# Optimization experiments

Measured on AMD Instinct MI355X. Metric: run time of the kernel, lower is better.

The kernel has to match this reference:

```python
import jax, jax.numpy as jnp
import numpy as np

N_NODES = 50000
N_EDGES = 800000
K_HOPS = 3


def setup_inputs() -> dict:
    key = jax.random.key(0)
    ks = jax.random.split(key, 8)
    x = jax.random.normal(ks[0], (N_NODES, 56), dtype=jnp.float32)
    edge_index = jax.random.randint(ks[1], (2, N_EDGES), 0, N_NODES, dtype=jnp.int64)
    def glorot(k, shape):
        fan_in, fan_out = shape
        s = (6.0 / (fan_in + fan_out)) ** 0.5
        return jax.random.uniform(k, shape, jnp.float32, -s, s)
    return {
        "x": x,
        "edge_index": edge_index,
        "W1": glorot(ks[2], (56, 64)), "b1": jnp.zeros((64,), jnp.float32),
        "W2": glorot(ks[3], (64, 64)), "b2": jnp.zeros((64,), jnp.float32),
        "W3": glorot(ks[4], (64, 64)), "b3": jnp.zeros((64,), jnp.float32),
        "W4": glorot(ks[5], (64, 256)), "b4": jnp.zeros((256,), jnp.float32),
    }


def _gcn_norm(edge_index, num_nodes, dtype):
    # add self loops (PyG SGConv default), then symmetric D^{-1/2}(A+I)D^{-1/2} weights
    loop = jnp.arange(num_nodes, dtype=edge_index.dtype)
    src = jnp.concatenate([edge_index[0], loop])
    dst = jnp.concatenate([edge_index[1], loop])
    deg = jax.ops.segment_sum(jnp.ones_like(src, dtype=dtype), dst, num_segments=num_nodes)
    dinv = jnp.where(deg > 0, jax.lax.rsqrt(deg), 0.0).astype(dtype)
    norm = dinv[src] * dinv[dst]  # [E + N]
    return src, dst, norm


def _propagate_k(h, src, dst, norm, num_nodes, k):
    # k hops of sparse gather-scale-scatter: h <- A_hat @ h
    for _ in range(k):
        h = jax.ops.segment_sum(h[src] * norm[:, None], dst, num_segments=num_nodes)
    return h


def reference(x, edge_index, W1, b1, W2, b2, W3, b3, W4, b4):
    n = x.shape[0]
    src, dst, norm = _gcn_norm(edge_index, n, x.dtype)
    # SGConv layers (dropout is identity in eval mode)
    h = _propagate_k(x, src, dst, norm, n, K_HOPS) @ W1 + b1
    h = _propagate_k(h, src, dst, norm, n, K_HOPS) @ W2 + b2
    h = _propagate_k(h, src, dst, norm, n, K_HOPS) @ W3 + b3
    return h @ W4 + b4  # [N, output]
```

## Files before the change

### kernel.cpp

```cpp
#include <hip/hip_runtime.h>

#define N_NODES 50000
#define N_EDGES 800000
#define F_IN 56
#define F_PAD 64
#define F_OUT 256
#define NB 32
#define ELL_W 64
#define SEG_SZ 6250
#define ZROW N_NODES


__global__ __launch_bounds__(256) void k_fill(const int* __restrict__ ei,
                                              int* __restrict__ cnt,
                                              int* __restrict__ ell) {
  int seg = blockIdx.x & 7;
  int chunk = blockIdx.x >> 3;
  int nchunks = gridDim.x >> 3;
  int stride = nchunks * blockDim.x;
  for (int e = chunk * blockDim.x + threadIdx.x; e < N_EDGES; e += stride) {
    int d = ei[N_EDGES + e];
    if (d / SEG_SZ == seg) {
      int s = ei[e];
      int pos = atomicAdd(&cnt[d], 1);
      ell[(d << 6) + pos] = s;
    }
  }
}


__global__ void k_prep(const int* __restrict__ cnt, float* __restrict__ dinv,
                       float* __restrict__ ideg, float* __restrict__ sqd,
                       int* __restrict__ deg, int* __restrict__ ell) {
  int i = blockIdx.x * blockDim.x + threadIdx.x;
  if (i >= N_NODES) return;
  int c = cnt[i] + 1;
  float fc = (float)c;
  dinv[i] = rsqrtf(fc);
  ideg[i] = 1.0f / fc;
  sqd[i]  = sqrtf(fc);
  deg[i] = c;
  ell[(i << 6) + (c - 1)] = i;
}


__global__ void k_loadx(const float* __restrict__ x, const float* __restrict__ dinv,
                        float* __restrict__ h) {
  int i = blockIdx.x * blockDim.x + threadIdx.x;
  int nn = i >> 6, f = i & 63;
  float di = dinv[nn];
  float v = 0.f;
  if (f < F_IN) v = x[nn * F_IN + f] * di;
  else if (f == F_IN) v = di;
  h[i] = v;
}


__global__ __launch_bounds__(256) void k_hop(const float* __restrict__ hin,
                                             float* __restrict__ hout,
                                             const int* __restrict__ deg,
                                             const int* __restrict__ ell,
                                             const float* __restrict__ ideg,
                                             float* __restrict__ vsave) {
  int node = (blockIdx.x * blockDim.x + threadIdx.x) >> 6;
  int lane = threadIdx.x & 63;
  int d = __builtin_amdgcn_readfirstlane(deg[node]);
  int rec = ell[((size_t)node << 6) + lane];
  rec = (lane < d) ? rec : ZROW;
  float idg = __int_as_float(__builtin_amdgcn_readfirstlane(
      __float_as_int(ideg[node])));

  int sub = lane >> 4;
  int fo  = (lane & 15) << 2;
  float4 acc = make_float4(0.f, 0.f, 0.f, 0.f);

  int ngroups = (d + 3) >> 2;
  int g = 0;
  for (; g + 4 <= ngroups; g += 4) {
    int s0 = __shfl(rec, g * 4 + sub);
    int s1 = __shfl(rec, g * 4 + 4 + sub);
    int s2 = __shfl(rec, g * 4 + 8 + sub);
    int s3 = __shfl(rec, g * 4 + 12 + sub);
    float4 a0 = *(const float4*)(hin + (((size_t)s0) << 6) + fo);
    float4 a1 = *(const float4*)(hin + (((size_t)s1) << 6) + fo);
    float4 a2 = *(const float4*)(hin + (((size_t)s2) << 6) + fo);
    float4 a3 = *(const float4*)(hin + (((size_t)s3) << 6) + fo);
    acc.x += (a0.x + a1.x) + (a2.x + a3.x);
    acc.y += (a0.y + a1.y) + (a2.y + a3.y);
    acc.z += (a0.z + a1.z) + (a2.z + a3.z);
    acc.w += (a0.w + a1.w) + (a2.w + a3.w);
  }
  for (; g < ngroups; ++g) {
    int s0 = __shfl(rec, g * 4 + sub);
    float4 a0 = *(const float4*)(hin + (((size_t)s0) << 6) + fo);
    acc.x += a0.x; acc.y += a0.y; acc.z += a0.z; acc.w += a0.w;
  }
  acc.x += __shfl_xor(acc.x, 16);
  acc.y += __shfl_xor(acc.y, 16);
  acc.z += __shfl_xor(acc.z, 16);
  acc.w += __shfl_xor(acc.w, 16);
  acc.x += __shfl_xor(acc.x, 32);
  acc.y += __shfl_xor(acc.y, 32);
  acc.z += __shfl_xor(acc.z, 32);
  acc.w += __shfl_xor(acc.w, 32);

  acc.x *= idg; acc.y *= idg; acc.z *= idg; acc.w *= idg;

  if (lane < 16) {
    *(float4*)(hout + ((size_t)node << 6) + fo) = acc;
  }
  if (vsave != nullptr && lane == 14) vsave[node] = acc.x;
}


__global__ void k_weights(const float* __restrict__ W1, const float* __restrict__ b1,
                          const float* __restrict__ W2, const float* __restrict__ b2,
                          const float* __restrict__ W3, const float* __restrict__ b3,
                          const float* __restrict__ W4, const float* __restrict__ b4,
                          float* __restrict__ Mw, float* __restrict__ c1,
                          float* __restrict__ c2, float* __restrict__ c3) {
  __shared__ float t1[64], t2[64], t3[64];
  int m = blockIdx.x, tid = threadIdx.x;
  if (m < F_IN) {
    if (tid < 64) {
      float a = 0.f;
      for (int k = 0; k < 64; ++k) a = fmaf(W1[m * 64 + k], W2[k * 64 + tid], a);
      t1[tid] = a;
    }
    __syncthreads();
    if (tid < 64) {
      float a = 0.f;
      for (int k = 0; k < 64; ++k) a = fmaf(t1[k], W3[k * 64 + tid], a);
      t2[tid] = a;
    }
    __syncthreads();
    {
      float a = 0.f;
      for (int k = 0; k < 64; ++k) a = fmaf(t2[k], W4[k * 256 + tid], a);
      Mw[m * 256 + tid] = a;
    }
  } else {
    if (tid < 64) {
      float a = 0.f;
      for (int k = 0; k < 64; ++k) a = fmaf(b1[k], W2[k * 64 + tid], a);
      t1[tid] = a;
    }
    __syncthreads();
    if (tid < 64) {
      float a = 0.f, b = 0.f;
      for (int k = 0; k < 64; ++k) {
        float w3 = W3[k * 64 + tid];
        a = fmaf(t1[k], w3, a);
        b = fmaf(b2[k], w3, b);
      }
      t2[tid] = a; t3[tid] = b;
    }
    __syncthreads();
    {
      float a = 0.f, b = 0.f, c = 0.f;
      for (int k = 0; k < 64; ++k) {
        float w4 = W4[k * 256 + tid];
        a = fmaf(t2[k], w4, a);
        b = fmaf(t3[k], w4, b);
        c = fmaf(b3[k], w4, c);
      }
      c1[tid] = a; c2[tid] = b; c3[tid] = c + b4[tid];
    }
  }
}


__global__ __launch_bounds__(256) void k_final(const float* __restrict__ y,
                                               const float* __restrict__ v3u,
                                               const float* __restrict__ v6u,
                                               const float* __restrict__ sqd,
                                               const float* __restrict__ Mw,
                                               const float* __restrict__ c1,
                                               const float* __restrict__ c2,
                                               const float* __restrict__ c3,
                                               float* __restrict__ out) {
  __shared__ float4 yl[NB][16];
  __shared__ float v3l[NB], v6l[NB];
  int tid = threadIdx.x;
  int j = tid;

  float4 Mreg[14];
#pragma unroll
  for (int k4 = 0; k4 < 14; ++k4) {
    Mreg[k4].x = Mw[(k4 * 4 + 0) * F_OUT + j];
    Mreg[k4].y = Mw[(k4 * 4 + 1) * F_OUT + j];
    Mreg[k4].z = Mw[(k4 * 4 + 2) * F_OUT + j];
    Mreg[k4].w = Mw[(k4 * 4 + 3) * F_OUT + j];
  }
  float C1 = c1[j], C2 = c2[j], C3 = c3[j];

  int n0 = blockIdx.x * NB;
  int lim = min(NB, N_NODES - n0);
  for (int i = tid; i < lim * 16; i += 256) {
    int nn = i >> 4, q = i & 15;
    float sq = sqd[n0 + nn];
    float4 v = *(const float4*)(y + ((size_t)(n0 + nn) << 6) + q * 4);
    v.x *= sq; v.y *= sq; v.z *= sq; v.w *= sq;
    yl[nn][q] = v;
  }
  if (tid < lim) {
    float sq = sqd[n0 + tid];
    v3l[tid] = v3u[n0 + tid] * sq;
    v6l[tid] = v6u[n0 + tid] * sq;
  }
  __syncthreads();

  for (int nn = 0; nn < lim; ++nn) {
    float a0 = fmaf(v6l[nn], C1, fmaf(v3l[nn], C2, C3));
    float a1 = 0.f, a2 = 0.f, a3 = 0.f;
#pragma unroll
    for (int k4 = 0; k4 < 14; ++k4) {
      float4 yv = yl[nn][k4];
      a0 = fmaf(yv.x, Mreg[k4].x, a0);
      a1 = fmaf(yv.y, Mreg[k4].y, a1);
      a2 = fmaf(yv.z, Mreg[k4].z, a2);
      a3 = fmaf(yv.w, Mreg[k4].w, a3);
    }
    out[(size_t)(n0 + nn) * F_OUT + j] = (a0 + a1) + (a2 + a3);
  }
}


extern "C" void kernel_launch(void* const* d_in, const int* in_sizes, int n_in,
                              void* d_out, int out_size, void* d_ws, size_t ws_size,
                              hipStream_t stream) {
  const float* x  = (const float*)d_in[0];
  const int*   ei = (const int*)d_in[1];
  const float* W1 = (const float*)d_in[2];
  const float* b1 = (const float*)d_in[3];
  const float* W2 = (const float*)d_in[4];
  const float* b2 = (const float*)d_in[5];
  const float* W3 = (const float*)d_in[6];
  const float* b3 = (const float*)d_in[7];
  const float* W4 = (const float*)d_in[8];
  const float* b4 = (const float*)d_in[9];
  float* out = (float*)d_out;

  char* ws = (char*)d_ws;
  size_t off = 0;
  auto take = [&](size_t bytes) -> void* {
    void* p = ws + off;
    off += (bytes + 255) & ~(size_t)255;
    return p;
  };
  int*   cnt   = (int*)take((size_t)N_NODES * 4);
  int*   deg   = (int*)take((size_t)N_NODES * 4);
  float* dinv  = (float*)take((size_t)N_NODES * 4);
  float* ideg  = (float*)take((size_t)N_NODES * 4);
  float* sqd   = (float*)take((size_t)N_NODES * 4);
  float* v3    = (float*)take((size_t)N_NODES * 4);
  float* v6    = (float*)take((size_t)N_NODES * 4);
  int*   ell   = (int*)take((size_t)N_NODES * ELL_W * 4);
  float* hA    = (float*)take((size_t)(N_NODES + 1) * F_PAD * 4);
  float* hB    = (float*)take((size_t)(N_NODES + 1) * F_PAD * 4);
  float* Mw    = (float*)take((size_t)F_IN * F_OUT * 4);
  float* c1    = (float*)take((size_t)F_OUT * 4);
  float* c2    = (float*)take((size_t)F_OUT * 4);
  float* c3    = (float*)take((size_t)F_OUT * 4);

  (void)hipMemsetAsync(cnt, 0, (size_t)N_NODES * 4, stream);
  (void)hipMemsetAsync(hA + (size_t)ZROW * F_PAD, 0, F_PAD * 4, stream);
  (void)hipMemsetAsync(hB + (size_t)ZROW * F_PAD, 0, F_PAD * 4, stream);
  k_fill<<<1024, 256, 0, stream>>>(ei, cnt, ell);
  k_prep<<<(N_NODES + 255) / 256, 256, 0, stream>>>(cnt, dinv, ideg, sqd, deg, ell);
  k_loadx<<<(N_NODES * F_PAD) / 256, 256, 0, stream>>>(x, dinv, hA);
  k_weights<<<F_IN + 1, 256, 0, stream>>>(W1, b1, W2, b2, W3, b3, W4, b4, Mw, c1, c2, c3);

  float* src = hA;
  float* dst = hB;
  for (int hop = 1; hop <= 9; ++hop) {
    float* vs = (hop == 3) ? v3 : (hop == 6) ? v6 : nullptr;
    k_hop<<<(N_NODES * F_PAD) / 256, 256, 0, stream>>>(src, dst, deg, ell, ideg, vs);
    float* t = src; src = dst; dst = t;
  }
  k_final<<<(N_NODES + NB - 1) / NB, 256, 0, stream>>>(src, v3, v6, sqd, Mw, c1, c2, c3, out);
}
```

Measured before the change: 363.3 us.

## Group four destination nodes per wavefront with sorted shared ELL lists

The per-node ELL layout (one wavefront per node, 64 slots) becomes a per-group layout in which four consecutive destination nodes share a 128-slot list. Each entry is tagged with its local destination, and a wavefront bitonic sort orders the entries by source. The hop kernel has one wavefront process a whole group, using all four 16-lane subgroups on useful edges instead of leaving padded lanes idle for low-degree nodes. Masked FMAs route each gathered row into four accumulators. This cuts wavefront count and wasted gathers, at the cost of four times the accumulate math, extra shuffle reductions, and a sort preprocessing pass.

```diff
diff --git a/kernel.cpp b/kernel.cpp
--- a/kernel.cpp
+++ b/kernel.cpp
@@ -2,18 +2,20 @@
 
 #define N_NODES 50000
 #define N_EDGES 800000
+#define N_GROUPS 12500
+#define GSLOTS 128
 #define F_IN 56
 #define F_PAD 64
 #define F_OUT 256
 #define NB 32
-#define ELL_W 64
 #define SEG_SZ 6250
 #define ZROW N_NODES
+#define PAD_E 0x7FFFFFFF
 
 
 __global__ __launch_bounds__(256) void k_fill(const int* __restrict__ ei,
-                                              int* __restrict__ cnt,
-                                              int* __restrict__ ell) {
+                                              int* __restrict__ gcnt,
+                                              int* __restrict__ ellg) {
   int seg = blockIdx.x & 7;
   int chunk = blockIdx.x >> 3;
   int nchunks = gridDim.x >> 3;
@@ -22,25 +24,74 @@
     int d = ei[N_EDGES + e];
     if (d / SEG_SZ == seg) {
       int s = ei[e];
-      int pos = atomicAdd(&cnt[d], 1);
-      ell[(d << 6) + pos] = s;
-    }
-  }
-}
-
-
-__global__ void k_prep(const int* __restrict__ cnt, float* __restrict__ dinv,
-                       float* __restrict__ ideg, float* __restrict__ sqd,
-                       int* __restrict__ deg, int* __restrict__ ell) {
+      int g = d >> 2;
+      int pos = atomicAdd(&gcnt[g], 1);
+      ellg[(g << 7) + pos] = (s << 2) | (d & 3);
+    }
+  }
+}
+
+
+__global__ void k_self(int* __restrict__ gcnt, int* __restrict__ ellg) {
   int i = blockIdx.x * blockDim.x + threadIdx.x;
   if (i >= N_NODES) return;
-  int c = cnt[i] + 1;
-  float fc = (float)c;
-  dinv[i] = rsqrtf(fc);
-  ideg[i] = 1.0f / fc;
-  sqd[i]  = sqrtf(fc);
-  deg[i] = c;
-  ell[(i << 6) + (c - 1)] = i;
+  int g = i >> 2;
+  int pos = atomicAdd(&gcnt[g], 1);
+  ellg[(g << 7) + pos] = (i << 2) | (i & 3);
+}
+
+
+__global__ __launch_bounds__(256) void k_sort(const int* __restrict__ gcnt,
+                                              int* __restrict__ ellg,
+                                              float* __restrict__ dinv,
+                                              float* __restrict__ ideg,
+                                              float* __restrict__ sqd) {
+  int w = (blockIdx.x * blockDim.x + threadIdx.x) >> 6;
+  int l = threadIdx.x & 63;
+  int cnt = __builtin_amdgcn_readfirstlane(gcnt[w]);
+  int* base = ellg + ((size_t)w << 7);
+  int v0 = (l < cnt) ? base[l] : PAD_E;
+  int v1 = (64 + l < cnt) ? base[64 + l] : PAD_E;
+
+#pragma unroll
+  for (int k = 2; k <= 128; k <<= 1) {
+#pragma unroll
+    for (int j = 64; j > 0; j >>= 1) {
+      if (j >= k) continue;
+      if (j == 64) {
+        int lo = min(v0, v1), hi = max(v0, v1);
+        v0 = lo; v1 = hi;
+      } else {
+        int o0 = __shfl_xor(v0, j);
+        int o1 = __shfl_xor(v1, j);
+        bool lower = ((l & j) == 0);
+        bool up0 = ((l & k) == 0);
+        bool up1 = (((l + 64) & k) == 0);
+        v0 = (lower == up0) ? min(v0, o0) : max(v0, o0);
+        v1 = (lower == up1) ? min(v1, o1) : max(v1, o1);
+      }
+    }
+  }
+
+  int c0 = __popcll(__ballot(v0 != PAD_E && (v0 & 3) == 0)) +
+           __popcll(__ballot(v1 != PAD_E && (v1 & 3) == 0));
+  int c1 = __popcll(__ballot(v0 != PAD_E && (v0 & 3) == 1)) +
+           __popcll(__ballot(v1 != PAD_E && (v1 & 3) == 1));
+  int c2 = __popcll(__ballot(v0 != PAD_E && (v0 & 3) == 2)) +
+           __popcll(__ballot(v1 != PAD_E && (v1 & 3) == 2));
+  int c3 = __popcll(__ballot(v0 != PAD_E && (v0 & 3) == 3)) +
+           __popcll(__ballot(v1 != PAD_E && (v1 & 3) == 3));
+  if (l < 4) {
+    int c = (l == 0) ? c0 : (l == 1) ? c1 : (l == 2) ? c2 : c3;
+    float fc = (float)c;
+    int node = (w << 2) + l;
+    dinv[node] = rsqrtf(fc);
+    ideg[node] = 1.0f / fc;
+    sqd[node]  = sqrtf(fc);
+  }
+
+  base[l] = (v0 == PAD_E) ? (ZROW << 2) : v0;
+  base[64 + l] = (v1 == PAD_E) ? (ZROW << 2) : v1;
 }
 
 
@@ -58,58 +109,72 @@
 
 __global__ __launch_bounds__(256) void k_hop(const float* __restrict__ hin,
                                              float* __restrict__ hout,
-                                             const int* __restrict__ deg,
-                                             const int* __restrict__ ell,
+                                             const int* __restrict__ gcnt,
+                                             const int* __restrict__ ellg,
                                              const float* __restrict__ ideg,
                                              float* __restrict__ vsave) {
-  int node = (blockIdx.x * blockDim.x + threadIdx.x) >> 6;
+  int w = (blockIdx.x * blockDim.x + threadIdx.x) >> 6;
   int lane = threadIdx.x & 63;
-  int d = __builtin_amdgcn_readfirstlane(deg[node]);
-  int rec = ell[((size_t)node << 6) + lane];
-  rec = (lane < d) ? rec : ZROW;
-  float idg = __int_as_float(__builtin_amdgcn_readfirstlane(
-      __float_as_int(ideg[node])));
-
-  int sub = lane >> 4;
-  int fo  = (lane & 15) << 2;
-  float4 acc = make_float4(0.f, 0.f, 0.f, 0.f);
-
-  int ngroups = (d + 3) >> 2;
+  int sub = lane >> 4, m = lane & 15, fo = m << 2;
+  int cnt = __builtin_amdgcn_readfirstlane(gcnt[w]);
+  const int* base = ellg + ((size_t)w << 7);
+  int rec0 = base[lane];
+  int rec1 = base[64 + lane];
+  float4 acc0 = make_float4(0.f, 0.f, 0.f, 0.f);
+  float4 acc1 = acc0, acc2 = acc0, acc3 = acc0;
+  int nq = (cnt + 3) >> 2;
+
+#define GATHER(IDX, EV, AV)                                          \
+  int EV = (IDX < 64) ? __shfl(rec0, IDX) : __shfl(rec1, IDX - 64);  \
+  float4 AV = *(const float4*)(hin + (((size_t)(EV >> 2)) << 6) + fo);
+
+#define ACCUM(EV, AV) {                                              \
+    int dd = EV & 3;                                                 \
+    float m0 = (dd == 0) ? 1.f : 0.f;                                \
+    float m1 = (dd == 1) ? 1.f : 0.f;                                \
+    float m2 = (dd == 2) ? 1.f : 0.f;                                \
+    float m3 = (dd == 3) ? 1.f : 0.f;                                \
+    acc0.x = fmaf(m0, AV.x, acc0.x); acc0.y = fmaf(m0, AV.y, acc0.y);\
+    acc0.z = fmaf(m0, AV.z, acc0.z); acc0.w = fmaf(m0, AV.w, acc0.w);\
+    acc1.x = fmaf(m1, AV.x, acc1.x); acc1.y = fmaf(m1, AV.y, acc1.y);\
+    acc1.z = fmaf(m1, AV.z, acc1.z); acc1.w = fmaf(m1, AV.w, acc1.w);\
+    acc2.x = fmaf(m2, AV.x, acc2.x); acc2.y = fmaf(m2, AV.y, acc2.y);\
+    acc2.z = fmaf(m2, AV.z, acc2.z); acc2.w = fmaf(m2, AV.w, acc2.w);\
+    acc3.x = fmaf(m3, AV.x, acc3.x); acc3.y = fmaf(m3, AV.y, acc3.y);\
+    acc3.z = fmaf(m3, AV.z, acc3.z); acc3.w = fmaf(m3, AV.w, acc3.w);\
+  }
+
   int g = 0;
-  for (; g + 4 <= ngroups; g += 4) {
-    int s0 = __shfl(rec, g * 4 + sub);
-    int s1 = __shfl(rec, g * 4 + 4 + sub);
-    int s2 = __shfl(rec, g * 4 + 8 + sub);
-    int s3 = __shfl(rec, g * 4 + 12 + sub);
-    float4 a0 = *(const float4*)(hin + (((size_t)s0) << 6) + fo);
-    float4 a1 = *(const float4*)(hin + (((size_t)s1) << 6) + fo);
-    float4 a2 = *(const float4*)(hin + (((size_t)s2) << 6) + fo);
-    float4 a3 = *(const float4*)(hin + (((size_t)s3) << 6) + fo);
-    acc.x += (a0.x + a1.x) + (a2.x + a3.x);
-    acc.y += (a0.y + a1.y) + (a2.y + a3.y);
-    acc.z += (a0.z + a1.z) + (a2.z + a3.z);
-    acc.w += (a0.w + a1.w) + (a2.w + a3.w);
-  }
-  for (; g < ngroups; ++g) {
-    int s0 = __shfl(rec, g * 4 + sub);
-    float4 a0 = *(const float4*)(hin + (((size_t)s0) << 6) + fo);
-    acc.x += a0.x; acc.y += a0.y; acc.z += a0.z; acc.w += a0.w;
-  }
-  acc.x += __shfl_xor(acc.x, 16);
-  acc.y += __shfl_xor(acc.y, 16);
-  acc.z += __shfl_xor(acc.z, 16);
-  acc.w += __shfl_xor(acc.w, 16);
-  acc.x += __shfl_xor(acc.x, 32);
-  acc.y += __shfl_xor(acc.y, 32);
-  acc.z += __shfl_xor(acc.z, 32);
-  acc.w += __shfl_xor(acc.w, 32);
-
-  acc.x *= idg; acc.y *= idg; acc.z *= idg; acc.w *= idg;
-
-  if (lane < 16) {
-    *(float4*)(hout + ((size_t)node << 6) + fo) = acc;
-  }
-  if (vsave != nullptr && lane == 14) vsave[node] = acc.x;
+  for (; g + 2 <= nq; g += 2) {
+    int i0 = (g << 2) + sub;
+    int i1 = i0 + 4;
+    GATHER(i0, e0, a0)
+    GATHER(i1, e1, a1)
+    ACCUM(e0, a0)
+    ACCUM(e1, a1)
+  }
+  if (g < nq) {
+    int i0 = (g << 2) + sub;
+    GATHER(i0, e0, a0)
+    ACCUM(e0, a0)
+  }
+#undef GATHER
+#undef ACCUM
+
+#define RED(A) \
+  A.x += __shfl_xor(A.x, 16); A.y += __shfl_xor(A.y, 16); \
+  A.z += __shfl_xor(A.z, 16); A.w += __shfl_xor(A.w, 16); \
+  A.x += __shfl_xor(A.x, 32); A.y += __shfl_xor(A.y, 32); \
+  A.z += __shfl_xor(A.z, 32); A.w += __shfl_xor(A.w, 32);
+  RED(acc0) RED(acc1) RED(acc2) RED(acc3)
+#undef RED
+
+  float4 v = (sub == 0) ? acc0 : (sub == 1) ? acc1 : (sub == 2) ? acc2 : acc3;
+  int node = (w << 2) + sub;
+  float idg = ideg[node];
+  v.x *= idg; v.y *= idg; v.z *= idg; v.w *= idg;
+  *(float4*)(hout + (((size_t)node) << 6) + fo) = v;
+  if (vsave != nullptr && m == 14) vsave[node] = v.x;
 }
 
 
@@ -248,14 +313,13 @@
     off += (bytes + 255) & ~(size_t)255;
     return p;
   };
-  int*   cnt   = (int*)take((size_t)N_NODES * 4);
-  int*   deg   = (int*)take((size_t)N_NODES * 4);
+  int*   gcnt  = (int*)take((size_t)N_GROUPS * 4);
   float* dinv  = (float*)take((size_t)N_NODES * 4);
   float* ideg  = (float*)take((size_t)N_NODES * 4);
   float* sqd   = (float*)take((size_t)N_NODES * 4);
   float* v3    = (float*)take((size_t)N_NODES * 4);
   float* v6    = (float*)take((size_t)N_NODES * 4);
-  int*   ell   = (int*)take((size_t)N_NODES * ELL_W * 4);
+  int*   ellg  = (int*)take((size_t)N_GROUPS * GSLOTS * 4);
   float* hA    = (float*)take((size_t)(N_NODES + 1) * F_PAD * 4);
   float* hB    = (float*)take((size_t)(N_NODES + 1) * F_PAD * 4);
   float* Mw    = (float*)take((size_t)F_IN * F_OUT * 4);
@@ -263,11 +327,12 @@
   float* c2    = (float*)take((size_t)F_OUT * 4);
   float* c3    = (float*)take((size_t)F_OUT * 4);
 
-  (void)hipMemsetAsync(cnt, 0, (size_t)N_NODES * 4, stream);
+  (void)hipMemsetAsync(gcnt, 0, (size_t)N_GROUPS * 4, stream);
   (void)hipMemsetAsync(hA + (size_t)ZROW * F_PAD, 0, F_PAD * 4, stream);
   (void)hipMemsetAsync(hB + (size_t)ZROW * F_PAD, 0, F_PAD * 4, stream);
-  k_fill<<<1024, 256, 0, stream>>>(ei, cnt, ell);
-  k_prep<<<(N_NODES + 255) / 256, 256, 0, stream>>>(cnt, dinv, ideg, sqd, deg, ell);
+  k_fill<<<1024, 256, 0, stream>>>(ei, gcnt, ellg);
+  k_self<<<(N_NODES + 255) / 256, 256, 0, stream>>>(gcnt, ellg);
+  k_sort<<<(N_GROUPS * 64) / 256, 256, 0, stream>>>(gcnt, ellg, dinv, ideg, sqd);
   k_loadx<<<(N_NODES * F_PAD) / 256, 256, 0, stream>>>(x, dinv, hA);
   k_weights<<<F_IN + 1, 256, 0, stream>>>(W1, b1, W2, b2, W3, b3, W4, b4, Mw, c1, c2, c3);
 
@@ -275,7 +340,7 @@
   float* dst = hB;
   for (int hop = 1; hop <= 9; ++hop) {
     float* vs = (hop == 3) ? v3 : (hop == 6) ? v6 : nullptr;
-    k_hop<<<(N_NODES * F_PAD) / 256, 256, 0, stream>>>(src, dst, deg, ell, ideg, vs);
+    k_hop<<<(N_GROUPS * 64) / 256, 256, 0, stream>>>(src, dst, gcnt, ellg, ideg, vs);
     float* t = src; src = dst; dst = t;
   }
   k_final<<<(N_NODES + NB - 1) / NB, 256, 0, stream>>>(src, v3, v6, sqd, Mw, c1, c2, c3, out);
```

Result: no change. 357.6 us (-1.6%).

## Slice features into XCD-local 16-wide panels with persistent hop kernel and 16-bit ELL

Applied to the files above, without the earlier changes.

Stores node features as four slices of 16 floats and maps hop blocks so that each slice is handled by blocks on a fixed pair of XCDs (by blockIdx & 7). Each slice of about 3.2 MB can then stay in one XCD's L2 during the gather. The hop kernel becomes grid-stride and persistent, processing four nodes per wave, using nontemporal stores for its outputs. Neighbor indices shrink to unsigned short to halve ELL traffic. k_final is restructured with NB=16 and register accumulators. This relies on the block-to-XCD round-robin dispatch and on node ids fitting in 16 bits, and it adds some lane imbalance when node degrees within a wave differ.

```diff
diff --git a/kernel.cpp b/kernel.cpp
--- a/kernel.cpp
+++ b/kernel.cpp
@@ -2,18 +2,26 @@
 
 #define N_NODES 50000
 #define N_EDGES 800000
+#define N_GROUPS 12500
+#define ELL_W 64
 #define F_IN 56
 #define F_PAD 64
 #define F_OUT 256
-#define NB 32
-#define ELL_W 64
+#define NB 16
 #define SEG_SZ 6250
 #define ZROW N_NODES
+#define NSL 4
+#define ROW_F 16
+#define SL_STRIDE ((size_t)(N_NODES + 1) * ROW_F)
+#define HOP_BLOCKS 624
+#define WAVES_PER_SLICE 624
+
+typedef float f32x4 __attribute__((ext_vector_type(4)));
 
 
 __global__ __launch_bounds__(256) void k_fill(const int* __restrict__ ei,
                                               int* __restrict__ cnt,
-                                              int* __restrict__ ell) {
+                                              unsigned short* __restrict__ ell) {
   int seg = blockIdx.x & 7;
   int chunk = blockIdx.x >> 3;
   int nchunks = gridDim.x >> 3;
@@ -23,93 +31,114 @@
     if (d / SEG_SZ == seg) {
       int s = ei[e];
       int pos = atomicAdd(&cnt[d], 1);
-      ell[(d << 6) + pos] = s;
-    }
-  }
-}
-
-
-__global__ void k_prep(const int* __restrict__ cnt, float* __restrict__ dinv,
-                       float* __restrict__ ideg, float* __restrict__ sqd,
-                       int* __restrict__ deg, int* __restrict__ ell) {
+      ell[((size_t)d << 6) + pos] = (unsigned short)s;
+    }
+  }
+}
+
+
+__global__ void k_prep(const int* __restrict__ cnt, int* __restrict__ deg,
+                       unsigned short* __restrict__ ell, float* __restrict__ dinv,
+                       float* __restrict__ ideg, float* __restrict__ sqd) {
   int i = blockIdx.x * blockDim.x + threadIdx.x;
   if (i >= N_NODES) return;
-  int c = cnt[i] + 1;
-  float fc = (float)c;
+  int c = cnt[i];
+  int d = c + 1;
+  ell[((size_t)i << 6) + c] = (unsigned short)i;
+  deg[i] = d;
+  float fc = (float)d;
   dinv[i] = rsqrtf(fc);
   ideg[i] = 1.0f / fc;
   sqd[i]  = sqrtf(fc);
-  deg[i] = c;
-  ell[(i << 6) + (c - 1)] = i;
 }
 
 
 __global__ void k_loadx(const float* __restrict__ x, const float* __restrict__ dinv,
-                        float* __restrict__ h) {
+                        float* __restrict__ hA, float* __restrict__ hB) {
   int i = blockIdx.x * blockDim.x + threadIdx.x;
-  int nn = i >> 6, f = i & 63;
-  float di = dinv[nn];
+  if (i >= (N_NODES + 1) * 64) return;
+  int node = i >> 6, f = i & 63;
+  int s = f >> 4, fi = f & 15;
+  size_t addr = (size_t)s * SL_STRIDE + ((size_t)node << 4) + fi;
+  if (node == N_NODES) {
+    hA[addr] = 0.f;
+    hB[addr] = 0.f;
+    return;
+  }
+  float di = dinv[node];
   float v = 0.f;
-  if (f < F_IN) v = x[nn * F_IN + f] * di;
+  if (f < F_IN) v = x[node * F_IN + f] * di;
   else if (f == F_IN) v = di;
-  h[i] = v;
-}
-
-
-__global__ __launch_bounds__(256) void k_hop(const float* __restrict__ hin,
-                                             float* __restrict__ hout,
+  hA[addr] = v;
+}
+
+
+__global__ __launch_bounds__(256) void k_hop(const float* __restrict__ hA_all,
+                                             float* __restrict__ hB_all,
                                              const int* __restrict__ deg,
-                                             const int* __restrict__ ell,
+                                             const unsigned short* __restrict__ ell,
                                              const float* __restrict__ ideg,
                                              float* __restrict__ vsave) {
-  int node = (blockIdx.x * blockDim.x + threadIdx.x) >> 6;
+  int bid = blockIdx.x;
+  int xslot = bid & 7;
+  int slice = xslot >> 1;
+  int ws = ((bid >> 3) << 1) + (xslot & 1);
+  int wv = (ws << 2) + (threadIdx.x >> 6);
   int lane = threadIdx.x & 63;
-  int d = __builtin_amdgcn_readfirstlane(deg[node]);
-  int rec = ell[((size_t)node << 6) + lane];
-  rec = (lane < d) ? rec : ZROW;
-  float idg = __int_as_float(__builtin_amdgcn_readfirstlane(
-      __float_as_int(ideg[node])));
-
-  int sub = lane >> 4;
-  int fo  = (lane & 15) << 2;
-  float4 acc = make_float4(0.f, 0.f, 0.f, 0.f);
-
-  int ngroups = (d + 3) >> 2;
-  int g = 0;
-  for (; g + 4 <= ngroups; g += 4) {
-    int s0 = __shfl(rec, g * 4 + sub);
-    int s1 = __shfl(rec, g * 4 + 4 + sub);
-    int s2 = __shfl(rec, g * 4 + 8 + sub);
-    int s3 = __shfl(rec, g * 4 + 12 + sub);
-    float4 a0 = *(const float4*)(hin + (((size_t)s0) << 6) + fo);
-    float4 a1 = *(const float4*)(hin + (((size_t)s1) << 6) + fo);
-    float4 a2 = *(const float4*)(hin + (((size_t)s2) << 6) + fo);
-    float4 a3 = *(const float4*)(hin + (((size_t)s3) << 6) + fo);
-    acc.x += (a0.x + a1.x) + (a2.x + a3.x);
-    acc.y += (a0.y + a1.y) + (a2.y + a3.y);
-    acc.z += (a0.z + a1.z) + (a2.z + a3.z);
-    acc.w += (a0.w + a1.w) + (a2.w + a3.w);
-  }
-  for (; g < ngroups; ++g) {
-    int s0 = __shfl(rec, g * 4 + sub);
-    float4 a0 = *(const float4*)(hin + (((size_t)s0) << 6) + fo);
-    acc.x += a0.x; acc.y += a0.y; acc.z += a0.z; acc.w += a0.w;
-  }
-  acc.x += __shfl_xor(acc.x, 16);
-  acc.y += __shfl_xor(acc.y, 16);
-  acc.z += __shfl_xor(acc.z, 16);
-  acc.w += __shfl_xor(acc.w, 16);
-  acc.x += __shfl_xor(acc.x, 32);
-  acc.y += __shfl_xor(acc.y, 32);
-  acc.z += __shfl_xor(acc.z, 32);
-  acc.w += __shfl_xor(acc.w, 32);
-
-  acc.x *= idg; acc.y *= idg; acc.z *= idg; acc.w *= idg;
-
-  if (lane < 16) {
-    *(float4*)(hout + ((size_t)node << 6) + fo) = acc;
-  }
-  if (vsave != nullptr && lane == 14) vsave[node] = acc.x;
+  int n2 = lane >> 4, sub = (lane >> 2) & 3, fq = lane & 3;
+  const float* __restrict__ hin = hA_all + (size_t)slice * SL_STRIDE;
+  float* __restrict__ hout = hB_all + (size_t)slice * SL_STRIDE;
+  bool do_v = (vsave != nullptr) && (slice == 3);
+
+  for (int g = wv; g < N_GROUPS; g += WAVES_PER_SLICE) {
+    int node = (g << 2) + n2;
+    int d = deg[node];
+    int dmax = max(d, __shfl_xor(d, 16));
+    dmax = max(dmax, __shfl_xor(dmax, 32));
+    int nq = (dmax + 3) >> 2;
+    const unsigned short* row = ell + ((size_t)node << 6);
+    float4 acc = make_float4(0.f, 0.f, 0.f, 0.f);
+
+#define CH(K, EV, AV)                                                     \
+    int ei_##EV = ((c + K) << 2) + sub;                                   \
+    int EV = (ei_##EV < d) ? (int)row[ei_##EV] : ZROW;                    \
+    float4 AV = *(const float4*)(hin + ((size_t)EV << 4) + (fq << 2));
+#define AC(AV) { acc.x += AV.x; acc.y += AV.y; acc.z += AV.z; acc.w += AV.w; }
+
+    int c = 0;
+    for (; c + 4 <= nq; c += 4) {
+      CH(0, e0, a0)
+      CH(1, e1, a1)
+      CH(2, e2, a2)
+      CH(3, e3, a3)
+      AC(a0) AC(a1) AC(a2) AC(a3)
+    }
+    for (; c < nq; ++c) {
+      CH(0, e0, a0)
+      AC(a0)
+    }
+#undef CH
+#undef AC
+
+    acc.x += __shfl_xor(acc.x, 4);
+    acc.y += __shfl_xor(acc.y, 4);
+    acc.z += __shfl_xor(acc.z, 4);
+    acc.w += __shfl_xor(acc.w, 4);
+    acc.x += __shfl_xor(acc.x, 8);
+    acc.y += __shfl_xor(acc.y, 8);
+    acc.z += __shfl_xor(acc.z, 8);
+    acc.w += __shfl_xor(acc.w, 8);
+
+    float idg = ideg[node];
+    acc.x *= idg; acc.y *= idg; acc.z *= idg; acc.w *= idg;
+
+    if (sub == 0) {
+      f32x4 av; av.x = acc.x; av.y = acc.y; av.z = acc.z; av.w = acc.w;
+      __builtin_nontemporal_store(av,
+          (f32x4*)(hout + ((size_t)node << 4) + (fq << 2)));
+      if (do_v && fq == 2) vsave[node] = acc.x;
+    }
+  }
 }
 
 
@@ -195,34 +224,43 @@
   float C1 = c1[j], C2 = c2[j], C3 = c3[j];
 
   int n0 = blockIdx.x * NB;
-  int lim = min(NB, N_NODES - n0);
-  for (int i = tid; i < lim * 16; i += 256) {
-    int nn = i >> 4, q = i & 15;
+  {
+    int nn = tid >> 4, q = tid & 15;
+    int s = q >> 2, qq = q & 3;
     float sq = sqd[n0 + nn];
-    float4 v = *(const float4*)(y + ((size_t)(n0 + nn) << 6) + q * 4);
+    float4 v = *(const float4*)(y + (size_t)s * SL_STRIDE +
+                                ((size_t)(n0 + nn) << 4) + (qq << 2));
     v.x *= sq; v.y *= sq; v.z *= sq; v.w *= sq;
     yl[nn][q] = v;
   }
-  if (tid < lim) {
+  if (tid < NB) {
     float sq = sqd[n0 + tid];
     v3l[tid] = v3u[n0 + tid] * sq;
     v6l[tid] = v6u[n0 + tid] * sq;
   }
   __syncthreads();
 
-  for (int nn = 0; nn < lim; ++nn) {
-    float a0 = fmaf(v6l[nn], C1, fmaf(v3l[nn], C2, C3));
-    float a1 = 0.f, a2 = 0.f, a3 = 0.f;
-#pragma unroll
-    for (int k4 = 0; k4 < 14; ++k4) {
+  float acc[NB];
+#pragma unroll
+  for (int nn = 0; nn < NB; ++nn)
+    acc[nn] = fmaf(v6l[nn], C1, fmaf(v3l[nn], C2, C3));
+
+#pragma unroll
+  for (int k4 = 0; k4 < 14; ++k4) {
+    float4 mk = Mreg[k4];
+#pragma unroll
+    for (int nn = 0; nn < NB; ++nn) {
       float4 yv = yl[nn][k4];
-      a0 = fmaf(yv.x, Mreg[k4].x, a0);
-      a1 = fmaf(yv.y, Mreg[k4].y, a1);
-      a2 = fmaf(yv.z, Mreg[k4].z, a2);
-      a3 = fmaf(yv.w, Mreg[k4].w, a3);
-    }
-    out[(size_t)(n0 + nn) * F_OUT + j] = (a0 + a1) + (a2 + a3);
-  }
+      acc[nn] = fmaf(yv.w, mk.w,
+                fmaf(yv.z, mk.z,
+                fmaf(yv.y, mk.y,
+                fmaf(yv.x, mk.x, acc[nn]))));
+    }
+  }
+
+#pragma unroll
+  for (int nn = 0; nn < NB; ++nn)
+    out[(size_t)(n0 + nn) * F_OUT + j] = acc[nn];
 }
 
 
@@ -248,35 +286,33 @@
     off += (bytes + 255) & ~(size_t)255;
     return p;
   };
-  int*   cnt   = (int*)take((size_t)N_NODES * 4);
-  int*   deg   = (int*)take((size_t)N_NODES * 4);
-  float* dinv  = (float*)take((size_t)N_NODES * 4);
-  float* ideg  = (float*)take((size_t)N_NODES * 4);
-  float* sqd   = (float*)take((size_t)N_NODES * 4);
-  float* v3    = (float*)take((size_t)N_NODES * 4);
-  float* v6    = (float*)take((size_t)N_NODES * 4);
-  int*   ell   = (int*)take((size_t)N_NODES * ELL_W * 4);
-  float* hA    = (float*)take((size_t)(N_NODES + 1) * F_PAD * 4);
-  float* hB    = (float*)take((size_t)(N_NODES + 1) * F_PAD * 4);
-  float* Mw    = (float*)take((size_t)F_IN * F_OUT * 4);
-  float* c1    = (float*)take((size_t)F_OUT * 4);
-  float* c2    = (float*)take((size_t)F_OUT * 4);
-  float* c3    = (float*)take((size_t)F_OUT * 4);
+  int*            cnt  = (int*)take((size_t)N_NODES * 4);
+  int*            deg  = (int*)take((size_t)N_NODES * 4);
+  float*          dinv = (float*)take((size_t)N_NODES * 4);
+  float*          ideg = (float*)take((size_t)N_NODES * 4);
+  float*          sqd  = (float*)take((size_t)N_NODES * 4);
+  float*          v3   = (float*)take((size_t)N_NODES * 4);
+  float*          v6   = (float*)take((size_t)N_NODES * 4);
+  unsigned short* ell  = (unsigned short*)take((size_t)N_NODES * ELL_W * 2);
+  float*          hA   = (float*)take(SL_STRIDE * NSL * 4);
+  float*          hB   = (float*)take(SL_STRIDE * NSL * 4);
+  float*          Mw   = (float*)take((size_t)F_IN * F_OUT * 4);
+  float*          c1   = (float*)take((size_t)F_OUT * 4);
+  float*          c2   = (float*)take((size_t)F_OUT * 4);
+  float*          c3   = (float*)take((size_t)F_OUT * 4);
 
   (void)hipMemsetAsync(cnt, 0, (size_t)N_NODES * 4, stream);
-  (void)hipMemsetAsync(hA + (size_t)ZROW * F_PAD, 0, F_PAD * 4, stream);
-  (void)hipMemsetAsync(hB + (size_t)ZROW * F_PAD, 0, F_PAD * 4, stream);
-  k_fill<<<1024, 256, 0, stream>>>(ei, cnt, ell);
-  k_prep<<<(N_NODES + 255) / 256, 256, 0, stream>>>(cnt, dinv, ideg, sqd, deg, ell);
-  k_loadx<<<(N_NODES * F_PAD) / 256, 256, 0, stream>>>(x, dinv, hA);
+  k_fill<<<512, 256, 0, stream>>>(ei, cnt, ell);
+  k_prep<<<(N_NODES + 255) / 256, 256, 0, stream>>>(cnt, deg, ell, dinv, ideg, sqd);
+  k_loadx<<<((N_NODES + 1) * 64 + 255) / 256, 256, 0, stream>>>(x, dinv, hA, hB);
   k_weights<<<F_IN + 1, 256, 0, stream>>>(W1, b1, W2, b2, W3, b3, W4, b4, Mw, c1, c2, c3);
 
   float* src = hA;
   float* dst = hB;
   for (int hop = 1; hop <= 9; ++hop) {
     float* vs = (hop == 3) ? v3 : (hop == 6) ? v6 : nullptr;
-    k_hop<<<(N_NODES * F_PAD) / 256, 256, 0, stream>>>(src, dst, deg, ell, ideg, vs);
+    k_hop<<<HOP_BLOCKS, 256, 0, stream>>>(src, dst, deg, ell, ideg, vs);
     float* t = src; src = dst; dst = t;
   }
-  k_final<<<(N_NODES + NB - 1) / NB, 256, 0, stream>>>(src, v3, v6, sqd, Mw, c1, c2, c3, out);
-}
+  k_final<<<N_NODES / NB, 256, 0, stream>>>(src, v3, v6, sqd, Mw, c1, c2, c3, out);
+}
```

Result: slower. 670.7 us (+84.6%).
